# Performance work log

Hardware: AMD Instinct MI355X
Metric: run time of the kernel (lower is better)

Reference implementation:

```python
import jax, jax.numpy as jnp
import numpy as np

NUM_BLOCKS = 4

def _pos_encoding(S, E):
    pos = np.arange(S, dtype=np.float32)[:, None]
    div = np.exp(np.arange(0, E, 2, dtype=np.float32) * (-np.log(10000.0) / E))
    pe = np.zeros((S, E), np.float32)
    pe[:, 0::2] = np.sin(pos * div)
    pe[:, 1::2] = np.cos(pos * div)
    return jnp.asarray(pe)

def _quantum_marginals(rotation_params, E):
    # Circuit: per-wire RX(a) RY(b) RZ(c) on |0>, then CNOT chain.
    # Per-wire P(|1>) after rotations (RZ does not affect probabilities):
    a = rotation_params[:E]
    b = rotation_params[E:2 * E]
    ca, sa = jnp.cos(a / 2), jnp.sin(a / 2)
    cb, sb = jnp.cos(b / 2), jnp.sin(b / 2)
    p1 = (sb * ca) ** 2 + (cb * sa) ** 2
    # CNOT chain -> cumulative XOR of measurement bits; marginal recursion:
    def step(q, p):
        qn = q + p - 2.0 * q * p
        return qn, qn
    q0 = p1[0]
    _, rest = jax.lax.scan(step, q0, p1[1:])
    return jnp.concatenate([q0[None], rest])  # [E]

def setup_inputs() -> dict:
    key = jax.random.key(0)
    ks = jax.random.split(key, 10)
    V, E, F, B, S = 32000, 1024, 4096, 8, 2048
    return {
        "input_ids": jax.random.randint(ks[0], (B, S), 0, V),
        "rotation_params": jax.random.normal(ks[1], (3 * E,), jnp.float32),
        "entangle_params": jax.random.normal(ks[2], (E - 1,), jnp.float32),
        "emb_table": jax.random.normal(ks[3], (V, E), jnp.float32) * 0.02,
        "ffn1_w": jax.random.normal(ks[4], (F, E), jnp.float32) / np.sqrt(E).astype(np.float32),
        "ffn1_b": jnp.zeros((F,), jnp.float32),
        "ffn2_w": jax.random.normal(ks[5], (E, F), jnp.float32) / np.sqrt(F).astype(np.float32),
        "ffn2_b": jnp.zeros((E,), jnp.float32),
        "clf_w": jax.random.normal(ks[6], (1, E), jnp.float32) / np.sqrt(E).astype(np.float32),
        "clf_b": jnp.zeros((1,), jnp.float32),
    }

def reference(input_ids, rotation_params, entangle_params, emb_table,
              ffn1_w, ffn1_b, ffn2_w, ffn2_b, clf_w, clf_b):
    B, S = input_ids.shape
    E = emb_table.shape[1]
    # Embedding + positional encoding (faithful, though overwritten by the
    # quantum block as in the original module, whose circuit ignores `inputs`).
    x = emb_table[input_ids] + _pos_encoding(S, E)
    qv = _quantum_marginals(rotation_params, E)  # same for every token/batch
    for _ in range(NUM_BLOCKS):
        x = jnp.broadcast_to(qv, (B, S, E))
        h = jax.nn.relu(jnp.einsum('bse,fe->bsf', x, ffn1_w) + ffn1_b)
        x = jnp.einsum('bsf,ef->bse', h, ffn2_w) + ffn2_b
    x = x.mean(axis=1)  # [B, E]
    return x @ clf_w.T + clf_b  # [B, 1]
```

## Files before the change

### kernel.cpp

```cpp
#include <hip/hip_runtime.h>
#include <stdint.h>


#define EDIM 1024
#define FDIM 4096
#define NBLK 256
#define TPB  1024
#define FB   16

__global__ __launch_bounds__(TPB) void fused_main(
    const float* __restrict__ rot,
    const float* __restrict__ ffn1_w,
    const float* __restrict__ ffn1_b,
    const float* __restrict__ ffn2_w,
    const float* __restrict__ clf_w,
    float* __restrict__ partials)
{
    __shared__ __align__(16) float qv_s[EDIM];
    __shared__ float wagg[16];
    __shared__ float h_s[FB];
    __shared__ float red[16];

    const int tid  = threadIdx.x;
    const int lane = tid & 63;
    const int wave = tid >> 6;
    const int d    = blockIdx.x;
    const int l    = ((d & 7) << 5) | (d >> 3);
    const int f0   = l * FB;

    const float* w1row = ffn1_w + (size_t)(f0 + wave) * EDIM;
    float4 w1[4];
#pragma unroll
    for (int it = 0; it < 4; ++it)
        w1[it] = *reinterpret_cast<const float4*>(w1row + it * 256 + lane * 4);

    const int c4 = tid & 3;
    const int g  = tid >> 2;
    float4 w2[4]; float cw[4];
#pragma unroll
    for (int k = 0; k < 4; ++k) {
        const int e = g + 256 * k;
        w2[k] = *reinterpret_cast<const float4*>(ffn2_w + (size_t)e * FDIM + f0 + 4 * c4);
        cw[k] = clf_w[e];
    }

    const float a = rot[tid];
    const float b = rot[EDIM + tid];

    const float r = cosf(a) * cosf(b);
    float v = r;
#pragma unroll
    for (int off = 1; off < 64; off <<= 1) {
        const float u = __shfl_up(v, off, 64);
        if (lane >= off) v *= u;
    }
    if (lane == 63) wagg[wave] = v;
    __syncthreads();
    float pre = 1.0f;
#pragma unroll
    for (int w = 0; w < 16; ++w)
        if (w < wave) pre *= wagg[w];
    qv_s[tid] = 0.5f * (1.0f - pre * v);
    __syncthreads();

    float4 acc4 = make_float4(0.f, 0.f, 0.f, 0.f);
#pragma unroll
    for (int k = 0; k < 4; ++k) {
        acc4.x += cw[k] * w2[k].x;
        acc4.y += cw[k] * w2[k].y;
        acc4.z += cw[k] * w2[k].z;
        acc4.w += cw[k] * w2[k].w;
    }

    const float4* qv4 = reinterpret_cast<const float4*>(qv_s);
    float s = 0.f;
#pragma unroll
    for (int it = 0; it < 4; ++it) {
        const float4 q4 = qv4[it * 64 + lane];
        s += w1[it].x * q4.x + w1[it].y * q4.y + w1[it].z * q4.z + w1[it].w * q4.w;
    }
#pragma unroll
    for (int off = 32; off; off >>= 1) s += __shfl_down(s, off, 64);
    if (lane == 0) h_s[wave] = fmaxf(s + ffn1_b[f0 + wave], 0.0f);
    __syncthreads();

    float p = acc4.x * h_s[4 * c4]     + acc4.y * h_s[4 * c4 + 1]
            + acc4.z * h_s[4 * c4 + 2] + acc4.w * h_s[4 * c4 + 3];
#pragma unroll
    for (int off = 32; off; off >>= 1) p += __shfl_down(p, off, 64);
    if (lane == 0) red[wave] = p;
    __syncthreads();
    if (tid == 0) {
        float t = 0.f;
#pragma unroll
        for (int w = 0; w < 16; ++w) t += red[w];
        partials[l] = t;
    }
}

__global__ __launch_bounds__(256) void finalize(
    const float* __restrict__ partials,
    const float* __restrict__ ffn2_b,
    const float* __restrict__ clf_w,
    const float* __restrict__ clf_b,
    float* __restrict__ out)
{
    __shared__ float red[4];
    const int tid = threadIdx.x, lane = tid & 63, wave = tid >> 6;
    float s = partials[tid];
    const float4 cwv = reinterpret_cast<const float4*>(clf_w)[tid];
    const float4 fbv = reinterpret_cast<const float4*>(ffn2_b)[tid];
    s += cwv.x * fbv.x + cwv.y * fbv.y + cwv.z * fbv.z + cwv.w * fbv.w;
#pragma unroll
    for (int off = 32; off; off >>= 1) s += __shfl_down(s, off, 64);
    if (lane == 0) red[wave] = s;
    __syncthreads();
    if (tid == 0) {
        const float t = red[0] + red[1] + red[2] + red[3] + clf_b[0];
#pragma unroll
        for (int b = 0; b < 8; ++b) out[b] = t;
    }
}

extern "C" void kernel_launch(void* const* d_in, const int* in_sizes, int n_in,
                              void* d_out, int out_size, void* d_ws, size_t ws_size,
                              hipStream_t stream) {
    (void)in_sizes; (void)n_in; (void)out_size; (void)ws_size;
    const float* rot    = (const float*)d_in[1];
    const float* ffn1_w = (const float*)d_in[4];
    const float* ffn1_b = (const float*)d_in[5];
    const float* ffn2_w = (const float*)d_in[6];
    const float* ffn2_b = (const float*)d_in[7];
    const float* clf_w  = (const float*)d_in[8];
    const float* clf_b  = (const float*)d_in[9];

    float* partials = (float*)d_ws;
    float* out = (float*)d_out;

    fused_main<<<NBLK, TPB, 0, stream>>>(rot, ffn1_w, ffn1_b, ffn2_w, clf_w, partials);
    finalize<<<1, 256, 0, stream>>>(partials, ffn2_b, clf_w, clf_b, out);
}
```

Measured before the change: 12.59 us.

## Split work into 512 smaller blocks and fold bias term into main kernel

Halves the threads per block and the FFN rows per block, doubling the grid to 512 blocks so more CUs share the weight streaming. Each thread now computes two elements of the cumulative-product scan, using an exclusive prefix. The ffn2_b·clf_w dot product moves from the finalize kernel into the per-block epilogue, and the clf-weighted w2 accumulation is placed after the first reduction. The aim is better CU coverage and less tail work in finalize, at the cost of recomputing the qv scan in twice as many blocks.

```diff
diff --git a/kernel.cpp b/kernel.cpp
--- a/kernel.cpp
+++ b/kernel.cpp
@@ -4,29 +4,33 @@
 
 #define EDIM 1024
 #define FDIM 4096
-#define NBLK 256
-#define TPB  1024
-#define FB   16
+#define NBLK 512
+#define TPB  512
+#define FB   8
 
 __global__ __launch_bounds__(TPB) void fused_main(
     const float* __restrict__ rot,
     const float* __restrict__ ffn1_w,
     const float* __restrict__ ffn1_b,
     const float* __restrict__ ffn2_w,
+    const float* __restrict__ ffn2_b,
     const float* __restrict__ clf_w,
     float* __restrict__ partials)
 {
     __shared__ __align__(16) float qv_s[EDIM];
-    __shared__ float wagg[16];
+    __shared__ float wagg[8];
     __shared__ float h_s[FB];
-    __shared__ float red[16];
+    __shared__ float red[8];
 
     const int tid  = threadIdx.x;
     const int lane = tid & 63;
     const int wave = tid >> 6;
     const int d    = blockIdx.x;
-    const int l    = ((d & 7) << 5) | (d >> 3);
+    const int l    = ((d & 7) << 6) | (d >> 3);
     const int f0   = l * FB;
+
+    const float2 a2 = *reinterpret_cast<const float2*>(rot + 2 * tid);
+    const float2 b2 = *reinterpret_cast<const float2*>(rot + EDIM + 2 * tid);
 
     const float* w1row = ffn1_w + (size_t)(f0 + wave) * EDIM;
     float4 w1[4];
@@ -34,43 +38,37 @@
     for (int it = 0; it < 4; ++it)
         w1[it] = *reinterpret_cast<const float4*>(w1row + it * 256 + lane * 4);
 
-    const int c4 = tid & 3;
-    const int g  = tid >> 2;
+    const int c2 = tid & 1;
+    const int g  = tid >> 1;
     float4 w2[4]; float cw[4];
 #pragma unroll
     for (int k = 0; k < 4; ++k) {
         const int e = g + 256 * k;
-        w2[k] = *reinterpret_cast<const float4*>(ffn2_w + (size_t)e * FDIM + f0 + 4 * c4);
+        w2[k] = *reinterpret_cast<const float4*>(ffn2_w + (size_t)e * FDIM + f0 + 4 * c2);
         cw[k] = clf_w[e];
     }
 
-    const float a = rot[tid];
-    const float b = rot[EDIM + tid];
-
-    const float r = cosf(a) * cosf(b);
-    float v = r;
+    const float r0 = cosf(a2.x) * cosf(b2.x);
+    const float r1 = cosf(a2.y) * cosf(b2.y);
+    const float pr = r0 * r1;
+    float v = pr;
 #pragma unroll
     for (int off = 1; off < 64; off <<= 1) {
         const float u = __shfl_up(v, off, 64);
         if (lane >= off) v *= u;
     }
+    const float vx = __shfl_up(v, 1, 64);
+    const float excl = (lane == 0) ? 1.0f : vx;
     if (lane == 63) wagg[wave] = v;
     __syncthreads();
     float pre = 1.0f;
 #pragma unroll
-    for (int w = 0; w < 16; ++w)
+    for (int w = 0; w < 8; ++w)
         if (w < wave) pre *= wagg[w];
-    qv_s[tid] = 0.5f * (1.0f - pre * v);
+    const float P = pre * excl;
+    qv_s[2 * tid]     = 0.5f * (1.0f - P * r0);
+    qv_s[2 * tid + 1] = 0.5f * (1.0f - P * pr);
     __syncthreads();
-
-    float4 acc4 = make_float4(0.f, 0.f, 0.f, 0.f);
-#pragma unroll
-    for (int k = 0; k < 4; ++k) {
-        acc4.x += cw[k] * w2[k].x;
-        acc4.y += cw[k] * w2[k].y;
-        acc4.z += cw[k] * w2[k].z;
-        acc4.w += cw[k] * w2[k].w;
-    }
 
     const float4* qv4 = reinterpret_cast<const float4*>(qv_s);
     float s = 0.f;
@@ -82,10 +80,19 @@
 #pragma unroll
     for (int off = 32; off; off >>= 1) s += __shfl_down(s, off, 64);
     if (lane == 0) h_s[wave] = fmaxf(s + ffn1_b[f0 + wave], 0.0f);
+
+    float4 acc4 = make_float4(0.f, 0.f, 0.f, 0.f);
+#pragma unroll
+    for (int k = 0; k < 4; ++k) {
+        acc4.x += cw[k] * w2[k].x;
+        acc4.y += cw[k] * w2[k].y;
+        acc4.z += cw[k] * w2[k].z;
+        acc4.w += cw[k] * w2[k].w;
+    }
     __syncthreads();
 
-    float p = acc4.x * h_s[4 * c4]     + acc4.y * h_s[4 * c4 + 1]
-            + acc4.z * h_s[4 * c4 + 2] + acc4.w * h_s[4 * c4 + 3];
+    float p = acc4.x * h_s[4 * c2]     + acc4.y * h_s[4 * c2 + 1]
+            + acc4.z * h_s[4 * c2 + 2] + acc4.w * h_s[4 * c2 + 3];
 #pragma unroll
     for (int off = 32; off; off >>= 1) p += __shfl_down(p, off, 64);
     if (lane == 0) red[wave] = p;
@@ -93,30 +100,30 @@
     if (tid == 0) {
         float t = 0.f;
 #pragma unroll
-        for (int w = 0; w < 16; ++w) t += red[w];
+        for (int w = 0; w < 8; ++w) t += red[w];
+        const float2 cwb = *reinterpret_cast<const float2*>(clf_w + 2 * l);
+        const float2 fbb = *reinterpret_cast<const float2*>(ffn2_b + 2 * l);
+        t += cwb.x * fbb.x + cwb.y * fbb.y;
         partials[l] = t;
     }
 }
 
-__global__ __launch_bounds__(256) void finalize(
+__global__ __launch_bounds__(TPB) void finalize(
     const float* __restrict__ partials,
-    const float* __restrict__ ffn2_b,
-    const float* __restrict__ clf_w,
     const float* __restrict__ clf_b,
     float* __restrict__ out)
 {
-    __shared__ float red[4];
+    __shared__ float red[8];
     const int tid = threadIdx.x, lane = tid & 63, wave = tid >> 6;
     float s = partials[tid];
-    const float4 cwv = reinterpret_cast<const float4*>(clf_w)[tid];
-    const float4 fbv = reinterpret_cast<const float4*>(ffn2_b)[tid];
-    s += cwv.x * fbv.x + cwv.y * fbv.y + cwv.z * fbv.z + cwv.w * fbv.w;
 #pragma unroll
     for (int off = 32; off; off >>= 1) s += __shfl_down(s, off, 64);
     if (lane == 0) red[wave] = s;
     __syncthreads();
     if (tid == 0) {
-        const float t = red[0] + red[1] + red[2] + red[3] + clf_b[0];
+        float t = clf_b[0];
+#pragma unroll
+        for (int w = 0; w < 8; ++w) t += red[w];
 #pragma unroll
         for (int b = 0; b < 8; ++b) out[b] = t;
     }
@@ -137,6 +144,7 @@
     float* partials = (float*)d_ws;
     float* out = (float*)d_out;
 
-    fused_main<<<NBLK, TPB, 0, stream>>>(rot, ffn1_w, ffn1_b, ffn2_w, clf_w, partials);
-    finalize<<<1, 256, 0, stream>>>(partials, ffn2_b, clf_w, clf_b, out);
+    fused_main<<<NBLK, TPB, 0, stream>>>(rot, ffn1_w, ffn1_b, ffn2_w, ffn2_b,
+                                         clf_w, partials);
+    finalize<<<1, TPB, 0, stream>>>(partials, clf_b, out);
 }
```

Result: slower. 12.87 us (+2.2%).
